# Optimization experiments

Hardware: AMD Instinct MI355X
Metric: run time of the kernel (lower is better)

The kernel has to match this reference:

```python
import jax, jax.numpy as jnp
import numpy as np
from jax import lax

D_MODEL = 384
D_INNER = 768          # expand * d_model
D_HALF = D_INNER // 2  # 384
D_STATE = 16
D_CONV = 4
DT_RANK = 24           # ceil(384/16)
BATCH = 8
SEQLEN = 4097
EXTRAS = 1
LMAIN = SEQLEN - EXTRAS


def setup_inputs() -> dict:
    key = jax.random.key(0)
    ks = jax.random.split(key, 12)
    hidden_states = jax.random.normal(ks[0], (BATCH, SEQLEN, D_MODEL), jnp.float32)
    in_proj_w = jax.random.normal(ks[1], (D_INNER, D_MODEL), jnp.float32) * 0.02
    conv_x_w = jax.random.normal(ks[2], (D_HALF, 1, D_CONV), jnp.float32) * 0.2
    conv_z_w = jax.random.normal(ks[3], (D_HALF, 1, D_CONV), jnp.float32) * 0.2
    x_proj_w = jax.random.normal(ks[4], (DT_RANK + 2 * D_STATE, D_HALF), jnp.float32) * 0.02
    dt_std = DT_RANK ** -0.5
    dt_proj_w = jax.random.uniform(ks[5], (D_HALF, DT_RANK), jnp.float32, -dt_std, dt_std)
    # bias = inverse softplus of dt sampled log-uniform in [1e-3, 1e-1]
    dt = jnp.exp(jax.random.uniform(ks[6], (D_HALF,), jnp.float32)
                 * (jnp.log(0.1) - jnp.log(0.001)) + jnp.log(0.001))
    dt = jnp.clip(dt, 1e-4, None)
    dt_proj_b = dt + jnp.log(-jnp.expm1(-dt))
    A_log = jnp.log(jnp.broadcast_to(jnp.arange(1, D_STATE + 1, dtype=jnp.float32),
                                     (D_HALF, D_STATE)))
    D_param = jnp.ones((D_HALF,), jnp.float32)
    out_proj_w = jax.random.normal(ks[7], (D_MODEL, D_HALF), jnp.float32) * 0.02
    perm = jax.random.permutation(ks[8], LMAIN).astype(jnp.int64)
    perm_rev = jnp.argsort(perm).astype(jnp.int64)
    return {
        "hidden_states": hidden_states,
        "in_proj_w": in_proj_w,
        "conv_x_w": conv_x_w,
        "conv_z_w": conv_z_w,
        "x_proj_w": x_proj_w,
        "dt_proj_w": dt_proj_w,
        "dt_proj_b": dt_proj_b,
        "A_log": A_log,
        "D_param": D_param,
        "out_proj_w": out_proj_w,
        "perm": perm,
        "perm_rev": perm_rev,
    }


def _depthwise_conv_same(x, w):
    # x: (B, C, L), w: (C, 1, K); torch padding='same' for k=4 -> pad (left=1, right=2)
    total = D_CONV - 1
    left = total // 2
    return lax.conv_general_dilated(
        x, w, window_strides=(1,), padding=[(left, total - left)],
        dimension_numbers=("NCH", "OIH", "NCH"), feature_group_count=D_HALF)


def _selective_scan(x, dt, A, Bm, Cm, D_param, delta_bias):
    # x, dt: (B, d, L); A: (d, n); Bm, Cm: (B, n, L)
    dt = jax.nn.softplus(dt + delta_bias[None, :, None])
    xT = jnp.moveaxis(x, 2, 0)    # (L, B, d)
    dtT = jnp.moveaxis(dt, 2, 0)  # (L, B, d)
    BT = jnp.moveaxis(Bm, 2, 0)   # (L, B, n)
    CT = jnp.moveaxis(Cm, 2, 0)   # (L, B, n)

    def step(h, inp):
        x_t, dt_t, B_t, C_t = inp
        dA = jnp.exp(dt_t[..., None] * A)                      # (B, d, n)
        h = h * dA + (dt_t * x_t)[..., None] * B_t[:, None, :]  # (B, d, n)
        y = jnp.einsum("bdn,bn->bd", h, C_t)
        return h, y

    h0 = jnp.zeros((x.shape[0], x.shape[1], A.shape[1]), x.dtype)
    _, ys = lax.scan(step, h0, (xT, dtT, BT, CT))
    y = jnp.moveaxis(ys, 0, 2)  # (B, d, L)
    return y + D_param[None, :, None] * x


def reference(hidden_states, in_proj_w, conv_x_w, conv_z_w, x_proj_w,
              dt_proj_w, dt_proj_b, A_log, D_param, out_proj_w, perm, perm_rev):
    # in_proj (no bias): (B,L,D) -> (B, d_inner, L)
    xz = jnp.einsum("bld,ed->bel", hidden_states, in_proj_w)
    # hilbert/zigzag reorder on the main (non-extra) tokens
    xz = jnp.concatenate([xz[:, :, :EXTRAS], xz[:, :, EXTRAS:][:, :, perm]], axis=2)

    x, z = jnp.split(xz, 2, axis=1)  # (B, d_half, L) each
    A = -jnp.exp(A_log)
    x = jax.nn.silu(_depthwise_conv_same(x, conv_x_w))
    z = jax.nn.silu(_depthwise_conv_same(z, conv_z_w))

    x_dbl = jnp.einsum("bdl,ed->bel", x, x_proj_w)  # (B, dt_rank+2n, L)
    dt_low, Bm, Cm = jnp.split(x_dbl, [DT_RANK, DT_RANK + D_STATE], axis=1)
    dt = jnp.einsum("brl,dr->bdl", dt_low, dt_proj_w)

    y = _selective_scan(x, dt, A, Bm, Cm, D_param, dt_proj_b)
    y = (y * z).transpose(0, 2, 1)  # (B, L, d_half)
    out = jnp.einsum("bld,ed->ble", y, out_proj_w)  # (B, L, D)
    # undo the permutation on the output
    out = jnp.concatenate([out[:, :EXTRAS], out[:, EXTRAS:][:, perm_rev]], axis=1)
    return out
```

## Files before the change

kernel.cpp:

```cpp
#include <hip/hip_runtime.h>
#include <hip/hip_bf16.h>

#define DEVI __device__ __forceinline__

constexpr int B_   = 8;
constexpr int L_   = 4097;
constexpr int MTOT = B_ * L_;
constexpr int DH   = 384;
constexpr int NS   = 16;
constexpr int CH   = 33;
constexpr int NCH  = (L_ + CH - 1) / CH;

typedef __bf16 bf16x8 __attribute__((ext_vector_type(8)));
typedef float  f32x4  __attribute__((ext_vector_type(4)));

DEVI float bl(unsigned v) { return __uint_as_float(v << 16); }
DEVI float bh(unsigned v) { return __uint_as_float(v & 0xffff0000u); }
DEVI float bf(const __hip_bfloat16 x) { return __bfloat162float(x); }
DEVI unsigned short f2bu(float x) {
  __hip_bfloat16 b = __float2bfloat16(x);
  return *(unsigned short*)&b;
}
DEVI float u16f(const uint4& u, int j) {
  const unsigned w = (&u.x)[j >> 1];
  return (j & 1) ? bh(w) : bl(w);
}
DEVI float softplus_f(float x) {
  return (x > 20.f) ? x : __logf(1.f + __expf(x));
}

DEVI void gld16(const __hip_bfloat16* g, __hip_bfloat16* l) {
  __builtin_amdgcn_global_load_lds(
      (const __attribute__((address_space(1))) void*)g,
      (__attribute__((address_space(3))) void*)l, 16, 0, 0);
}

__global__ void init_k(const void* hs, int* flagp,
                       const int* p0, const int* p1, int* d0, int* d1) {
  if (blockIdx.x == 0) {
    if (threadIdx.x == 0) {
      const unsigned short* u = (const unsigned short*)hs;
      int ok = 1;
      for (int i = 0; i < 8; ++i) {
        const unsigned short v = u[2 * i];
        const int e = (v >> 7) & 0xFF;
        if (!(v == 0 || (e >= 100 && e <= 140))) ok = 0;
      }
      flagp[0] = ok;
      flagp[1] = 1;
    }
    return;
  }
  __shared__ int s_or;
  const int* src = (blockIdx.x == 2) ? p1 : p0;
  int*       dst = (blockIdx.x == 2) ? d1 : d0;
  if (threadIdx.x == 0) s_or = 0;
  __syncthreads();
  int loc = 0;
  for (int i = threadIdx.x; i < 2048; i += 1024) loc |= src[2 * i + 1];
  atomicOr(&s_or, loc);
  __syncthreads();
  const bool is64 = (s_or == 0);
  for (int j = threadIdx.x; j < 4096; j += 1024)
    dst[j] = is64 ? (int)((const long long*)src)[j] : src[j];
}

struct NormSet { const void* src[8]; void* dst[8]; int n[8]; };
__global__ void norm_all(NormSet s, int* flagp,
                         const void* __restrict__ alog, float* __restrict__ a2fo) {
  const int f = flagp[0];
  if (blockIdx.x == 1152) {
    int ok = 1;
    for (int d = threadIdx.x; d < 384; d += 256) {
      float a2[16];
#pragma unroll
      for (int n = 0; n < 16; ++n) {
        const float v = f ? bf(((const __hip_bfloat16*)alog)[d * 16 + n])
                          : ((const float*)alog)[d * 16 + n];
        a2[n] = -1.4426950408889634f * __expf(v);
        a2fo[d * 16 + n] = a2[n];
      }
#pragma unroll
      for (int n = 1; n < 16; ++n) {
        const float ref = (float)(n + 1) * a2[0];
        if (fabsf(a2[n] - ref) > 1e-3f * fabsf(ref)) ok = 0;
      }
    }
    if (!ok) atomicAnd(&flagp[1], 0);
    return;
  }
  const int idx = blockIdx.x * 256 + threadIdx.x;
#pragma unroll
  for (int t = 0; t < 8; ++t) {
    if (idx < s.n[t]) {
      __hip_bfloat16* d = (__hip_bfloat16*)s.dst[t];
      if (f) d[idx] = ((const __hip_bfloat16*)s.src[t])[idx];
      else   d[idx] = __float2bfloat16(((const float*)s.src[t])[idx]);
    }
  }
}

__global__ void prep_k(const __hip_bfloat16* __restrict__ dtw,
                       const __hip_bfloat16* __restrict__ xw,
                       __hip_bfloat16* __restrict__ wcomb) {
  const int idx = blockIdx.x * 256 + threadIdx.x;
  if (idx >= 512 * 384) return;
  const int n = idx / 384, k = idx - n * 384;
  float v = 0.f;
  if (n < 384) {
#pragma unroll
    for (int r = 0; r < 24; ++r) v += bf(dtw[n * 24 + r]) * bf(xw[r * 384 + k]);
  } else if (n < 416) {
    v = bf(xw[(24 + n - 384) * 384 + k]);
  }
  wcomb[idx] = __float2bfloat16(v);
}

__global__ void cvt_k(const void* __restrict__ hs, __hip_bfloat16* __restrict__ dst,
                      const int* __restrict__ gidx, const int* __restrict__ flagp) {
  const int idx = blockIdx.x * 256 + threadIdx.x;
  if (idx >= MTOT * 48) return;
  const int j = idx % 48;
  const int r = idx / 48;
  const int b = r / L_, t = r - b * L_;
  const int src = b * L_ + (t == 0 ? 0 : 1 + gidx[t - 1]);
  uint4 o;
  if (flagp[0]) {
    o = *(const uint4*)((const __hip_bfloat16*)hs + (size_t)src * 384 + j * 8);
  } else {
    const float* f = (const float*)hs + (size_t)src * 384 + j * 8;
    const float4 f0 = *(const float4*)f;
    const float4 f1 = *(const float4*)(f + 4);
    o.x = f2bu(f0.x) | ((unsigned)f2bu(f0.y) << 16);
    o.y = f2bu(f0.z) | ((unsigned)f2bu(f0.w) << 16);
    o.z = f2bu(f1.x) | ((unsigned)f2bu(f1.y) << 16);
    o.w = f2bu(f1.z) | ((unsigned)f2bu(f1.w) << 16);
  }
  *(uint4*)(dst + (size_t)r * 384 + j * 8) = o;
}

template<int GATHER, int EPI>
__global__ __launch_bounds__(256, 4)
void gemm_k(const __hip_bfloat16* __restrict__ A, const __hip_bfloat16* __restrict__ W,
            void* __restrict__ e0, void* __restrict__ e1,
            const __hip_bfloat16* __restrict__ bias,
            const int* __restrict__ gidx, const int* __restrict__ flagp,
            int M, int N)
{
  __shared__ __align__(16) char smem[36864];
  __hip_bfloat16* lA = (__hip_bfloat16*)smem;
  __hip_bfloat16* lB = lA + 2 * 4096;
  const int tid  = threadIdx.x;
  const int lane = tid & 63;
  const int wv   = tid >> 6;
  const int wm   = wv >> 1, wn = wv & 1;
  const int lrow = lane & 15, quad = lane >> 4;
  const int fbf  = flagp[0];

  const int NT = gridDim.x;
  const int nblocks = NT * (int)gridDim.y;
  const int id = blockIdx.y * NT + blockIdx.x;
  const int q8 = nblocks >> 3, r8 = nblocks & 7;
  const int xcd = id & 7, slot = id >> 3;
  const int nid = (xcd < r8 ? xcd * (q8 + 1)
                            : r8 * (q8 + 1) + (xcd - r8) * q8) + slot;
  const int mt = nid / NT, nt = nid - mt * NT;

  const bool live = !(EPI == 1 && nt * 128 + wn * 64 >= 416);

  const __hip_bfloat16* aSrc[2];
  const __hip_bfloat16* bSrc[2];
#pragma unroll
  for (int p = 0; p < 2; ++p) {
    const int s   = p * 256 + tid;
    const int row = s >> 2;
    const int kc  = (s & 3) * 8;
    int r = mt * 128 + row;
    if (r >= M) r = M - 1;
    int src;
    if (GATHER) { const int b = r / L_, t = r - b * L_;
                  src = b * L_ + (t == 0 ? 0 : 1 + gidx[t - 1]); }
    else        { src = r; }
    aSrc[p] = A + (size_t)src * 384 + kc;
    bSrc[p] = W + (size_t)(nt * 128 + row) * 384 + kc;
  }

  auto stage = [&](int kt, int buf) {
#pragma unroll
    for (int p = 0; p < 2; ++p) {
      const int s = p * 256 + tid;
      gld16(aSrc[p] + kt * 32, &lA[buf * 4096 + s * 8]);
      gld16(bSrc[p] + kt * 32, &lB[buf * 4096 + s * 8]);
    }
  };

  f32x4 acc[4][4] = {};

  stage(0, 0);
  __syncthreads();

#pragma unroll
  for (int kt = 0; kt < 12; ++kt) {
    const int buf = kt & 1;
    if (kt < 11) stage(kt + 1, buf ^ 1);
    if (live) {
      bf16x8 af[4], bfr[4];
#pragma unroll
      for (int i = 0; i < 4; ++i)
        af[i] = *reinterpret_cast<const bf16x8*>(
            &lA[buf * 4096 + (wm * 64 + i * 16 + lrow) * 32 + quad * 8]);
#pragma unroll
      for (int j = 0; j < 4; ++j)
        bfr[j] = *reinterpret_cast<const bf16x8*>(
            &lB[buf * 4096 + (wn * 64 + j * 16 + lrow) * 32 + quad * 8]);
#pragma unroll
      for (int i = 0; i < 4; ++i)
#pragma unroll
        for (int j = 0; j < 4; ++j)
          acc[i][j] = __builtin_amdgcn_mfma_f32_16x16x32_bf16(af[i], bfr[j], acc[i][j], 0, 0, 0);
    }
    __syncthreads();
  }

  const int r0c = mt * 128;
  if (EPI == 1 && nt == 3) {
#pragma unroll
    for (int i = 0; i < 4; ++i) {
      const int row0 = r0c + wm * 64 + i * 16 + quad * 4;
#pragma unroll
      for (int j = 0; j < 4; ++j) {
        const int col = 384 + wn * 64 + j * 16 + lrow;
        if (col >= 416) continue;
#pragma unroll
        for (int rg = 0; rg < 4; ++rg) {
          const int r = row0 + rg;
          if (r >= M) continue;
          ((float*)e1)[(size_t)r * 32 + (col - 384)] = acc[i][j][rg];
        }
      }
    }
  } else if (EPI == 2 && !fbf) {
    float* lT = (float*)smem;
#pragma unroll
    for (int h = 0; h < 2; ++h) {
      __syncthreads();
      if (wn == h) {
#pragma unroll
        for (int i = 0; i < 4; ++i)
#pragma unroll
          for (int j = 0; j < 4; ++j)
#pragma unroll
            for (int rg = 0; rg < 4; ++rg)
              lT[(wm * 64 + i * 16 + quad * 4 + rg) * 72 + j * 16 + lrow] = acc[i][j][rg];
      }
      __syncthreads();
#pragma unroll
      for (int p = 0; p < 8; ++p) {
        const int ch = p * 256 + tid;
        const int row = ch >> 4, c4 = (ch & 15) * 4;
        const int r = r0c + row;
        if (r < M) {
          const float4 v = *(const float4*)&lT[row * 72 + c4];
          *(float4*)((float*)e0 + (size_t)r * 384 + nt * 128 + h * 64 + c4) = v;
        }
      }
    }
  } else {
    __hip_bfloat16* lT = (__hip_bfloat16*)smem;
#pragma unroll
    for (int h = 0; h < 2; ++h) {
      __syncthreads();
      if (wn == h) {
        float bj[4] = {};
        if (EPI == 1) {
#pragma unroll
          for (int j = 0; j < 4; ++j)
            bj[j] = bf(bias[nt * 128 + h * 64 + j * 16 + lrow]);
        }
#pragma unroll
        for (int i = 0; i < 4; ++i)
#pragma unroll
          for (int j = 0; j < 4; ++j)
#pragma unroll
            for (int rg = 0; rg < 4; ++rg) {
              float v = acc[i][j][rg];
              if (EPI == 1) v = softplus_f(v + bj[j]);
              lT[(wm * 64 + i * 16 + quad * 4 + rg) * 72 + j * 16 + lrow] =
                  __float2bfloat16(v);
            }
      }
      __syncthreads();
#pragma unroll
      for (int p = 0; p < 4; ++p) {
        const int ch = p * 256 + tid;
        const int row = ch >> 3, c8 = (ch & 7) * 8;
        const int r = r0c + row;
        if (r < M) {
          const uint4 v = *(const uint4*)&lT[row * 72 + c8];
          const int g = nt * 128 + h * 64 + c8;
          __hip_bfloat16* dst = (EPI == 0 && g >= 384)
                ? (__hip_bfloat16*)e1 + (size_t)r * 384 + (g - 384)
                : (__hip_bfloat16*)e0 + (size_t)r * 384 + g;
          *(uint4*)dst = v;
        }
      }
    }
  }
}

__global__ void convx_k(const __hip_bfloat16* __restrict__ xh,
                        const __hip_bfloat16* __restrict__ cxw,
                        __hip_bfloat16* __restrict__ xc) {
  const int idx = blockIdx.x * 256 + threadIdx.x;
  if (idx >= MTOT * 48) return;
  const int g  = idx % 48;
  const int rg = idx / 48;
  const int t  = rg % L_;
  const int c0 = g * 8;
  uint4 wv[4];
#pragma unroll
  for (int p = 0; p < 4; ++p) wv[p] = *(const uint4*)(cxw + c0 * 4 + p * 8);
  float acc[8] = {};
#pragma unroll
  for (int k = 0; k < 4; ++k) {
    const int tt = t + k - 1;
    if (tt < 0 || tt >= L_) continue;
    const uint4 u = *(const uint4*)(xh + (size_t)(rg + k - 1) * 384 + c0);
#pragma unroll
    for (int j = 0; j < 8; ++j) {
      const int e = j * 4 + k;
      acc[j] += u16f(wv[e >> 3], e & 7) * u16f(u, j);
    }
  }
  uint4 o;
#pragma unroll
  for (int p = 0; p < 4; ++p) {
    const float s0 = acc[2 * p]     / (1.f + __expf(-acc[2 * p]));
    const float s1 = acc[2 * p + 1] / (1.f + __expf(-acc[2 * p + 1]));
    (&o.x)[p] = f2bu(s0) | ((unsigned)f2bu(s1) << 16);
  }
  *(uint4*)(xc + (size_t)rg * 384 + c0) = o;
}

__global__ __launch_bounds__(128)
void scan1_k(const __hip_bfloat16* __restrict__ dt, const float* __restrict__ bc,
             __hip_bfloat16* __restrict__ xcio,
             const float* __restrict__ a2f,
             const __hip_bfloat16* __restrict__ dpar,
             float* __restrict__ pbuf, float* __restrict__ hend,
             const int* __restrict__ flagp)
{
  __shared__ __align__(16) float lBC[CH * 32];
  const int blk = blockIdx.x;
  const int dt3 = blk % 3;
  const int c   = (blk / 3) % NCH;
  const int b   = blk / (3 * NCH);
  const int d   = dt3 * 128 + threadIdx.x;
  const int t0  = c * CH;
  const int r0  = b * L_ + t0;
  const int tmax = (L_ - t0 < CH) ? (L_ - t0) : CH;
  for (int i = threadIdx.x; i < tmax * 32; i += 128) lBC[i] = bc[(size_t)r0 * 32 + i];
  __syncthreads();

  float h[16];
#pragma unroll
  for (int n = 0; n < 16; ++n) h[n] = 0.f;
  float sdt = 0.f;
  const float Dd = bf(dpar[d]);
  const size_t base = ((size_t)(c * 8 + b) * 16) * 384 + d;

  float dtv = bf(dt[(size_t)r0 * 384 + d]);
  float xv  = bf(xcio[(size_t)r0 * 384 + d]);

  if (flagp[1]) {
    const float a2b = a2f[d * 16];
    for (int tt = 0; tt < tmax; ++tt) {
      const size_t r = (size_t)(r0 + tt);
      float dtv_n = 0.f, xv_n = 0.f;
      if (tt + 1 < tmax) {
        dtv_n = bf(dt[(r + 1) * 384 + d]);
        xv_n  = bf(xcio[(r + 1) * 384 + d]);
      }
      sdt += dtv;
      const float dtx = dtv * xv;
      float pw[17];
      pw[1] = exp2f(dtv * a2b);
#pragma unroll
      for (int n = 2; n <= 16; ++n) pw[n] = pw[n >> 1] * pw[n - (n >> 1)];
      float4 bq[4], cq[4];
#pragma unroll
      for (int q = 0; q < 4; ++q) {
        bq[q] = *(const float4*)&lBC[tt * 32 + q * 4];
        cq[q] = *(const float4*)&lBC[tt * 32 + 16 + q * 4];
      }
      float ya = 0.f, yb = 0.f;
#pragma unroll
      for (int n = 0; n < 16; ++n) {
        h[n] = h[n] * pw[n + 1] + dtx * (&bq[n >> 2].x)[n & 3];
        const float t = h[n] * (&cq[n >> 2].x)[n & 3];
        if (n & 1) yb += t; else ya += t;
      }
      const float y = ya + yb + Dd * xv;
      xcio[r * 384 + d] = __float2bfloat16(y);
      dtv = dtv_n; xv = xv_n;
    }
    float Ep[17];
    Ep[1] = exp2f(sdt * a2b);
#pragma unroll
    for (int n = 2; n <= 16; ++n) Ep[n] = Ep[n >> 1] * Ep[n - (n >> 1)];
#pragma unroll
    for (int n = 0; n < 16; ++n) {
      pbuf[base + n * 384] = Ep[n + 1];
      hend[base + n * 384] = h[n];
    }
  } else {
    float a2[16];
#pragma unroll
    for (int n = 0; n < 16; ++n) a2[n] = a2f[d * 16 + n];
    for (int tt = 0; tt < tmax; ++tt) {
      const size_t r = (size_t)(r0 + tt);
      float dtv_n = 0.f, xv_n = 0.f;
      if (tt + 1 < tmax) {
        dtv_n = bf(dt[(r + 1) * 384 + d]);
        xv_n  = bf(xcio[(r + 1) * 384 + d]);
      }
      sdt += dtv;
      const float dtx = dtv * xv;
      float4 bq[4], cq[4];
#pragma unroll
      for (int q = 0; q < 4; ++q) {
        bq[q] = *(const float4*)&lBC[tt * 32 + q * 4];
        cq[q] = *(const float4*)&lBC[tt * 32 + 16 + q * 4];
      }
      float ya = 0.f, yb = 0.f;
#pragma unroll
      for (int n = 0; n < 16; ++n) {
        h[n] = h[n] * exp2f(dtv * a2[n]) + dtx * (&bq[n >> 2].x)[n & 3];
        const float t = h[n] * (&cq[n >> 2].x)[n & 3];
        if (n & 1) yb += t; else ya += t;
      }
      const float y = ya + yb + Dd * xv;
      xcio[r * 384 + d] = __float2bfloat16(y);
      dtv = dtv_n; xv = xv_n;
    }
#pragma unroll
    for (int n = 0; n < 16; ++n) {
      pbuf[base + n * 384] = exp2f(sdt * a2[n]);
      hend[base + n * 384] = h[n];
    }
  }
}

__global__ void scan2_k(float* __restrict__ pbuf, const float* __restrict__ hend) {
  const int tid = blockIdx.x * 256 + threadIdx.x;
  const int d = tid % 384;
  const int n = (tid / 384) & 15;
  const int b = tid / 6144;
  float H = 0.f;
  for (int c = 0; c < NCH; ++c) {
    const size_t idx = ((size_t)(c * 8 + b) * 16 + n) * 384 + d;
    const float p = pbuf[idx];
    const float he = hend[idx];
    pbuf[idx] = H;
    H = p * H + he;
  }
}

__global__ __launch_bounds__(128)
void scan3_k(__hip_bfloat16* __restrict__ dtyg, const float* __restrict__ bc,
             const __hip_bfloat16* __restrict__ yl,
             const __hip_bfloat16* __restrict__ zh,
             const __hip_bfloat16* __restrict__ czw,
             const float* __restrict__ a2f,
             const float* __restrict__ hstart,
             const int* __restrict__ flagp)
{
  __shared__ __align__(16) float lC[CH * 16];
  const int blk = blockIdx.x;
  const int dt3 = blk % 3;
  const int c   = (blk / 3) % NCH;
  const int b   = blk / (3 * NCH);
  const int d   = dt3 * 128 + threadIdx.x;
  const int t0  = c * CH;
  const int r0  = b * L_ + t0;
  const int tmax = (L_ - t0 < CH) ? (L_ - t0) : CH;
  for (int i = threadIdx.x; i < tmax * 16; i += 128)
    lC[i] = bc[(size_t)r0 * 32 + (i >> 4) * 32 + 16 + (i & 15)];
  __syncthreads();

  float hs_[16];
  const size_t base = ((size_t)(c * 8 + b) * 16) * 384 + d;
#pragma unroll
  for (int n = 0; n < 16; ++n) hs_[n] = hstart[base + n * 384];
  float cw[4];
#pragma unroll
  for (int k = 0; k < 4; ++k) cw[k] = bf(czw[d * 4 + k]);

  float zm1 = (t0 - 1 >= 0) ? bf(zh[(size_t)(r0 - 1) * 384 + d]) : 0.f;
  float z0  = bf(zh[(size_t)r0 * 384 + d]);
  float zp1 = (t0 + 1 < L_) ? bf(zh[(size_t)(r0 + 1) * 384 + d]) : 0.f;
  float sdt = 0.f;

  float dtv = bf(dtyg[(size_t)r0 * 384 + d]);
  float ylv = bf(yl[(size_t)r0 * 384 + d]);

  if (flagp[1]) {
    const float a2b = a2f[d * 16];
    for (int tt = 0; tt < tmax; ++tt) {
      const int t = t0 + tt;
      const size_t r = (size_t)(r0 + tt);
      const float zp2 = (t + 2 < L_) ? bf(zh[(r + 2) * 384 + d]) : 0.f;
      float dtv_n = 0.f, ylv_n = 0.f;
      if (tt + 1 < tmax) {
        dtv_n = bf(dtyg[(r + 1) * 384 + d]);
        ylv_n = bf(yl[(r + 1) * 384 + d]);
      }
      sdt += dtv;
      float pw[17];
      pw[1] = exp2f(sdt * a2b);
#pragma unroll
      for (int n = 2; n <= 16; ++n) pw[n] = pw[n >> 1] * pw[n - (n >> 1)];
      float4 cq[4];
#pragma unroll
      for (int q = 0; q < 4; ++q) cq[q] = *(const float4*)&lC[tt * 16 + q * 4];
      float ca = 0.f, cb = 0.f;
#pragma unroll
      for (int n = 0; n < 16; ++n) {
        const float t2 = (&cq[n >> 2].x)[n & 3] * hs_[n] * pw[n + 1];
        if (n & 1) cb += t2; else ca += t2;
      }
      const float y = ylv + ca + cb;
      const float zc = cw[0] * zm1 + cw[1] * z0 + cw[2] * zp1 + cw[3] * zp2;
      const float zs = zc / (1.f + __expf(-zc));
      dtyg[r * 384 + d] = __float2bfloat16(y * zs);
      zm1 = z0; z0 = zp1; zp1 = zp2;
      dtv = dtv_n; ylv = ylv_n;
    }
  } else {
    float a2[16];
#pragma unroll
    for (int n = 0; n < 16; ++n) a2[n] = a2f[d * 16 + n];
    for (int tt = 0; tt < tmax; ++tt) {
      const int t = t0 + tt;
      const size_t r = (size_t)(r0 + tt);
      const float zp2 = (t + 2 < L_) ? bf(zh[(r + 2) * 384 + d]) : 0.f;
      float dtv_n = 0.f, ylv_n = 0.f;
      if (tt + 1 < tmax) {
        dtv_n = bf(dtyg[(r + 1) * 384 + d]);
        ylv_n = bf(yl[(r + 1) * 384 + d]);
      }
      sdt += dtv;
      float4 cq[4];
#pragma unroll
      for (int q = 0; q < 4; ++q) cq[q] = *(const float4*)&lC[tt * 16 + q * 4];
      float ca = 0.f, cb = 0.f;
#pragma unroll
      for (int n = 0; n < 16; ++n) {
        const float t2 = (&cq[n >> 2].x)[n & 3] * hs_[n] * exp2f(sdt * a2[n]);
        if (n & 1) cb += t2; else ca += t2;
      }
      const float y = ylv + ca + cb;
      const float zc = cw[0] * zm1 + cw[1] * z0 + cw[2] * zp1 + cw[3] * zp2;
      const float zs = zc / (1.f + __expf(-zc));
      dtyg[r * 384 + d] = __float2bfloat16(y * zs);
      zm1 = z0; z0 = zp1; zp1 = zp2;
      dtv = dtv_n; ylv = ylv_n;
    }
  }
}

extern "C" void kernel_launch(void* const* d_in, const int* in_sizes, int n_in,
                              void* d_out, int out_size, void* d_ws, size_t ws_size,
                              hipStream_t stream) {
  const void* hs   = d_in[0];
  const void* w_in = d_in[1];
  const void* cxw  = d_in[2];
  const void* czw  = d_in[3];
  const void* xw   = d_in[4];
  const void* dtw  = d_in[5];
  const void* dtb  = d_in[6];
  const void* alog = d_in[7];
  const void* dpar = d_in[8];
  const void* ow   = d_in[9];
  const int* perm  = (const int*)d_in[10];
  const int* permr = (const int*)d_in[11];

  char* ws = (char*)d_ws;
  size_t off = 0;
  auto alloc = [&](size_t nbytes) -> char* {
    char* p = ws + off;
    off += (nbytes + 255) & ~(size_t)255;
    return p;
  };
  int* flag              = (int*)alloc(256);
  int* nperm             = (int*)alloc(4096 * 4);
  int* npermr            = (int*)alloc(4096 * 4);
  float* a2f             = (float*)alloc(6144 * 4);
  __hip_bfloat16* w_inb  = (__hip_bfloat16*)alloc(294912 * 2);
  __hip_bfloat16* cxwb   = (__hip_bfloat16*)alloc(1536 * 2);
  __hip_bfloat16* czwb   = (__hip_bfloat16*)alloc(1536 * 2);
  __hip_bfloat16* xwb    = (__hip_bfloat16*)alloc(21504 * 2);
  __hip_bfloat16* dtwb   = (__hip_bfloat16*)alloc(9216 * 2);
  __hip_bfloat16* dtbb   = (__hip_bfloat16*)alloc(384 * 2);
  __hip_bfloat16* dparb  = (__hip_bfloat16*)alloc(384 * 2);
  __hip_bfloat16* owb    = (__hip_bfloat16*)alloc(147456 * 2);
  __hip_bfloat16* wcombb = (__hip_bfloat16*)alloc((size_t)512 * 384 * 2);
  __hip_bfloat16* hsb    = (__hip_bfloat16*)alloc((size_t)MTOT * 384 * 2);
  __hip_bfloat16* zh     = (__hip_bfloat16*)alloc((size_t)MTOT * 384 * 2);
  __hip_bfloat16* xc     = (__hip_bfloat16*)alloc((size_t)MTOT * 384 * 2);
  __hip_bfloat16* dtyg   = (__hip_bfloat16*)alloc((size_t)MTOT * 384 * 2);
  float*          bcf    = (float*)alloc((size_t)MTOT * 32 * 4);
  __hip_bfloat16* xh   = (__hip_bfloat16*)d_out;
  float*          pbuf = (float*)d_out;
  float*          hend = (float*)((char*)d_out + (size_t)NCH * B_ * NS * DH * 4);

  init_k<<<3, 1024, 0, stream>>>(hs, flag, perm, permr, nperm, npermr);
  NormSet ns;
  ns.src[0] = w_in; ns.dst[0] = w_inb; ns.n[0] = 294912;
  ns.src[1] = ow;   ns.dst[1] = owb;   ns.n[1] = 147456;
  ns.src[2] = xw;   ns.dst[2] = xwb;   ns.n[2] = 21504;
  ns.src[3] = dtw;  ns.dst[3] = dtwb;  ns.n[3] = 9216;
  ns.src[4] = cxw;  ns.dst[4] = cxwb;  ns.n[4] = 1536;
  ns.src[5] = czw;  ns.dst[5] = czwb;  ns.n[5] = 1536;
  ns.src[6] = dtb;  ns.dst[6] = dtbb;  ns.n[6] = 384;
  ns.src[7] = dpar; ns.dst[7] = dparb; ns.n[7] = 384;
  norm_all<<<1153, 256, 0, stream>>>(ns, flag, alog, a2f);
  prep_k<<<768, 256, 0, stream>>>(dtwb, xwb, wcombb);
  cvt_k<<<(MTOT * 48 + 255) / 256, 256, 0, stream>>>(hs, hsb, nperm, flag);
  gemm_k<0, 0><<<dim3(6, 257), 256, 0, stream>>>(
      hsb, w_inb, xh, zh, nullptr, nullptr, flag, MTOT, 768);
  convx_k<<<(MTOT * 48 + 255) / 256, 256, 0, stream>>>(xh, cxwb, xc);
  gemm_k<0, 1><<<dim3(4, 257), 256, 0, stream>>>(
      xc, wcombb, dtyg, bcf, dtbb, nullptr, flag, MTOT, 512);
  scan1_k<<<B_ * NCH * 3, 128, 0, stream>>>(dtyg, bcf, xc, a2f, dparb, pbuf, hend, flag);
  scan2_k<<<192, 256, 0, stream>>>(pbuf, hend);
  scan3_k<<<B_ * NCH * 3, 128, 0, stream>>>(dtyg, bcf, xc, zh, czwb, a2f, pbuf, flag);
  gemm_k<1, 2><<<dim3(3, 257), 256, 0, stream>>>(
      dtyg, owb, d_out, nullptr, nullptr, npermr, flag, MTOT, 384);
  (void)in_sizes; (void)n_in; (void)out_size; (void)ws_size;
}
```

Before: 334.4 us.

## Fuse input conversion and gather into in_proj GEMM; merge setup kernels

Removes the separate cvt_k pass, which gathered and converted the hidden states to a bf16 buffer. The in_proj GEMM now loads fp32 (or bf16) rows directly through registers with the permutation gather, converts them and writes them to LDS. It also merges init_k, norm_all and prep_k into one setup kernel that probes the dtype per block, cutting three launches to one. The trade-off is that the A operand no longer uses the async global_load_lds path, so the conversion adds register pressure and latency inside the GEMM loop.

```diff
diff --git a/kernel.cpp b/kernel.cpp
--- a/kernel.cpp
+++ b/kernel.cpp
@@ -28,6 +28,17 @@
 DEVI float softplus_f(float x) {
   return (x > 20.f) ? x : __logf(1.f + __expf(x));
 }
+DEVI int probe_bf16(const void* hs) {
+  const unsigned short* u = (const unsigned short*)hs;
+  int ok = 1;
+#pragma unroll
+  for (int i = 0; i < 8; ++i) {
+    const unsigned short v = u[2 * i];
+    const int e = (v >> 7) & 0xFF;
+    if (!(v == 0 || (e >= 100 && e <= 140))) ok = 0;
+  }
+  return ok;
+}
 
 DEVI void gld16(const __hip_bfloat16* g, __hip_bfloat16* l) {
   __builtin_amdgcn_global_load_lds(
@@ -35,41 +46,32 @@
       (__attribute__((address_space(3))) void*)l, 16, 0, 0);
 }
 
-__global__ void init_k(const void* hs, int* flagp,
-                       const int* p0, const int* p1, int* d0, int* d1) {
-  if (blockIdx.x == 0) {
-    if (threadIdx.x == 0) {
-      const unsigned short* u = (const unsigned short*)hs;
-      int ok = 1;
-      for (int i = 0; i < 8; ++i) {
-        const unsigned short v = u[2 * i];
-        const int e = (v >> 7) & 0xFF;
-        if (!(v == 0 || (e >= 100 && e <= 140))) ok = 0;
-      }
-      flagp[0] = ok;
-      flagp[1] = 1;
+struct NormSet { const void* src[6]; void* dst[6]; int n[6]; };
+__global__ void setup_k(const void* hs, int* flagp,
+                        const int* p0, const int* p1, int* d0, int* d1,
+                        NormSet s, const void* __restrict__ alog,
+                        float* __restrict__ a2fo,
+                        const void* __restrict__ dtw, const void* __restrict__ xw,
+                        __hip_bfloat16* __restrict__ wcomb) {
+  const int bid = blockIdx.x;
+  const int f = probe_bf16(hs);
+
+  if (bid < 1152) {
+    const int idx = bid * 256 + threadIdx.x;
+#pragma unroll
+    for (int t = 0; t < 6; ++t) {
+      if (idx < s.n[t]) {
+        __hip_bfloat16* d = (__hip_bfloat16*)s.dst[t];
+        if (f) d[idx] = ((const __hip_bfloat16*)s.src[t])[idx];
+        else   d[idx] = __float2bfloat16(((const float*)s.src[t])[idx]);
+      }
     }
     return;
   }
-  __shared__ int s_or;
-  const int* src = (blockIdx.x == 2) ? p1 : p0;
-  int*       dst = (blockIdx.x == 2) ? d1 : d0;
-  if (threadIdx.x == 0) s_or = 0;
-  __syncthreads();
-  int loc = 0;
-  for (int i = threadIdx.x; i < 2048; i += 1024) loc |= src[2 * i + 1];
-  atomicOr(&s_or, loc);
-  __syncthreads();
-  const bool is64 = (s_or == 0);
-  for (int j = threadIdx.x; j < 4096; j += 1024)
-    dst[j] = is64 ? (int)((const long long*)src)[j] : src[j];
-}
-
-struct NormSet { const void* src[8]; void* dst[8]; int n[8]; };
-__global__ void norm_all(NormSet s, int* flagp,
-                         const void* __restrict__ alog, float* __restrict__ a2fo) {
-  const int f = flagp[0];
-  if (blockIdx.x == 1152) {
+  if (bid == 1152) {
+    __shared__ int s_ok;
+    if (threadIdx.x == 0) s_ok = 1;
+    __syncthreads();
     int ok = 1;
     for (int d = threadIdx.x; d < 384; d += 256) {
       float a2[16];
@@ -86,62 +88,46 @@
         if (fabsf(a2[n] - ref) > 1e-3f * fabsf(ref)) ok = 0;
       }
     }
-    if (!ok) atomicAnd(&flagp[1], 0);
+    if (!ok) atomicAnd(&s_ok, 0);
+    __syncthreads();
+    if (threadIdx.x == 0) { flagp[0] = f; flagp[1] = s_ok; }
     return;
   }
-  const int idx = blockIdx.x * 256 + threadIdx.x;
-#pragma unroll
-  for (int t = 0; t < 8; ++t) {
-    if (idx < s.n[t]) {
-      __hip_bfloat16* d = (__hip_bfloat16*)s.dst[t];
-      if (f) d[idx] = ((const __hip_bfloat16*)s.src[t])[idx];
-      else   d[idx] = __float2bfloat16(((const float*)s.src[t])[idx]);
-    }
-  }
-}
-
-__global__ void prep_k(const __hip_bfloat16* __restrict__ dtw,
-                       const __hip_bfloat16* __restrict__ xw,
-                       __hip_bfloat16* __restrict__ wcomb) {
-  const int idx = blockIdx.x * 256 + threadIdx.x;
+  if (bid <= 1154) {
+    __shared__ int s_or;
+    const int* src = (bid == 1154) ? p1 : p0;
+    int*       dst = (bid == 1154) ? d1 : d0;
+    if (threadIdx.x == 0) s_or = 0;
+    __syncthreads();
+    int loc = 0;
+    for (int i = threadIdx.x; i < 2048; i += 256) loc |= src[2 * i + 1];
+    atomicOr(&s_or, loc);
+    __syncthreads();
+    const bool is64 = (s_or == 0);
+    for (int j = threadIdx.x; j < 4096; j += 256)
+      dst[j] = is64 ? (int)((const long long*)src)[j] : src[j];
+    return;
+  }
+  const int idx = (bid - 1155) * 256 + threadIdx.x;
   if (idx >= 512 * 384) return;
   const int n = idx / 384, k = idx - n * 384;
+  auto rd = [&](const void* w, int i) -> float {
+    return f ? bf(((const __hip_bfloat16*)w)[i])
+             : bf(__float2bfloat16(((const float*)w)[i]));
+  };
   float v = 0.f;
   if (n < 384) {
 #pragma unroll
-    for (int r = 0; r < 24; ++r) v += bf(dtw[n * 24 + r]) * bf(xw[r * 384 + k]);
+    for (int r = 0; r < 24; ++r) v += rd(dtw, n * 24 + r) * rd(xw, r * 384 + k);
   } else if (n < 416) {
-    v = bf(xw[(24 + n - 384) * 384 + k]);
+    v = rd(xw, (24 + n - 384) * 384 + k);
   }
   wcomb[idx] = __float2bfloat16(v);
 }
 
-__global__ void cvt_k(const void* __restrict__ hs, __hip_bfloat16* __restrict__ dst,
-                      const int* __restrict__ gidx, const int* __restrict__ flagp) {
-  const int idx = blockIdx.x * 256 + threadIdx.x;
-  if (idx >= MTOT * 48) return;
-  const int j = idx % 48;
-  const int r = idx / 48;
-  const int b = r / L_, t = r - b * L_;
-  const int src = b * L_ + (t == 0 ? 0 : 1 + gidx[t - 1]);
-  uint4 o;
-  if (flagp[0]) {
-    o = *(const uint4*)((const __hip_bfloat16*)hs + (size_t)src * 384 + j * 8);
-  } else {
-    const float* f = (const float*)hs + (size_t)src * 384 + j * 8;
-    const float4 f0 = *(const float4*)f;
-    const float4 f1 = *(const float4*)(f + 4);
-    o.x = f2bu(f0.x) | ((unsigned)f2bu(f0.y) << 16);
-    o.y = f2bu(f0.z) | ((unsigned)f2bu(f0.w) << 16);
-    o.z = f2bu(f1.x) | ((unsigned)f2bu(f1.y) << 16);
-    o.w = f2bu(f1.z) | ((unsigned)f2bu(f1.w) << 16);
-  }
-  *(uint4*)(dst + (size_t)r * 384 + j * 8) = o;
-}
-
-template<int GATHER, int EPI>
+template<int AFP, int GATHER, int EPI>
 __global__ __launch_bounds__(256, 4)
-void gemm_k(const __hip_bfloat16* __restrict__ A, const __hip_bfloat16* __restrict__ W,
+void gemm_k(const void* __restrict__ Av, const __hip_bfloat16* __restrict__ W,
             void* __restrict__ e0, void* __restrict__ e1,
             const __hip_bfloat16* __restrict__ bias,
             const int* __restrict__ gidx, const int* __restrict__ flagp,
@@ -168,7 +154,7 @@
 
   const bool live = !(EPI == 1 && nt * 128 + wn * 64 >= 416);
 
-  const __hip_bfloat16* aSrc[2];
+  size_t aOff[2];
   const __hip_bfloat16* bSrc[2];
 #pragma unroll
   for (int p = 0; p < 2; ++p) {
@@ -181,28 +167,67 @@
     if (GATHER) { const int b = r / L_, t = r - b * L_;
                   src = b * L_ + (t == 0 ? 0 : 1 + gidx[t - 1]); }
     else        { src = r; }
-    aSrc[p] = A + (size_t)src * 384 + kc;
+    aOff[p] = (size_t)src * 384 + kc;
     bSrc[p] = W + (size_t)(nt * 128 + row) * 384 + kc;
   }
 
-  auto stage = [&](int kt, int buf) {
+  float4 fA0[2], fA1[2];
+  uint4  uA[2];
+
+  auto issueA = [&](int kt) {
+    if (AFP) {
+      if (fbf) {
+#pragma unroll
+        for (int p = 0; p < 2; ++p)
+          uA[p] = *(const uint4*)((const __hip_bfloat16*)Av + aOff[p] + kt * 32);
+      } else {
+#pragma unroll
+        for (int p = 0; p < 2; ++p) {
+          const float* fp = (const float*)Av + aOff[p] + kt * 32;
+          fA0[p] = *(const float4*)fp;
+          fA1[p] = *(const float4*)(fp + 4);
+        }
+      }
+    }
+  };
+  auto writeA = [&](int buf) {
+    if (AFP) {
+#pragma unroll
+      for (int p = 0; p < 2; ++p) {
+        uint4 w;
+        if (fbf) {
+          w = uA[p];
+        } else {
+          w.x = f2bu(fA0[p].x) | ((unsigned)f2bu(fA0[p].y) << 16);
+          w.y = f2bu(fA0[p].z) | ((unsigned)f2bu(fA0[p].w) << 16);
+          w.z = f2bu(fA1[p].x) | ((unsigned)f2bu(fA1[p].y) << 16);
+          w.w = f2bu(fA1[p].z) | ((unsigned)f2bu(fA1[p].w) << 16);
+        }
+        *(uint4*)&lA[buf * 4096 + (p * 256 + tid) * 8] = w;
+      }
+    }
+  };
+  auto stageHW = [&](int kt, int buf) {
 #pragma unroll
     for (int p = 0; p < 2; ++p) {
       const int s = p * 256 + tid;
-      gld16(aSrc[p] + kt * 32, &lA[buf * 4096 + s * 8]);
+      if (!AFP)
+        gld16((const __hip_bfloat16*)Av + aOff[p] + kt * 32, &lA[buf * 4096 + s * 8]);
       gld16(bSrc[p] + kt * 32, &lB[buf * 4096 + s * 8]);
     }
   };
 
   f32x4 acc[4][4] = {};
 
-  stage(0, 0);
+  issueA(0);
+  stageHW(0, 0);
+  writeA(0);
   __syncthreads();
 
 #pragma unroll
   for (int kt = 0; kt < 12; ++kt) {
     const int buf = kt & 1;
-    if (kt < 11) stage(kt + 1, buf ^ 1);
+    if (kt < 11) { issueA(kt + 1); stageHW(kt + 1, buf ^ 1); }
     if (live) {
       bf16x8 af[4], bfr[4];
 #pragma unroll
@@ -219,6 +244,7 @@
         for (int j = 0; j < 4; ++j)
           acc[i][j] = __builtin_amdgcn_mfma_f32_16x16x32_bf16(af[i], bfr[j], acc[i][j], 0, 0, 0);
     }
+    if (kt < 11) writeA(buf ^ 1);
     __syncthreads();
   }
 
@@ -599,13 +625,10 @@
   __hip_bfloat16* w_inb  = (__hip_bfloat16*)alloc(294912 * 2);
   __hip_bfloat16* cxwb   = (__hip_bfloat16*)alloc(1536 * 2);
   __hip_bfloat16* czwb   = (__hip_bfloat16*)alloc(1536 * 2);
-  __hip_bfloat16* xwb    = (__hip_bfloat16*)alloc(21504 * 2);
-  __hip_bfloat16* dtwb   = (__hip_bfloat16*)alloc(9216 * 2);
   __hip_bfloat16* dtbb   = (__hip_bfloat16*)alloc(384 * 2);
   __hip_bfloat16* dparb  = (__hip_bfloat16*)alloc(384 * 2);
   __hip_bfloat16* owb    = (__hip_bfloat16*)alloc(147456 * 2);
   __hip_bfloat16* wcombb = (__hip_bfloat16*)alloc((size_t)512 * 384 * 2);
-  __hip_bfloat16* hsb    = (__hip_bfloat16*)alloc((size_t)MTOT * 384 * 2);
   __hip_bfloat16* zh     = (__hip_bfloat16*)alloc((size_t)MTOT * 384 * 2);
   __hip_bfloat16* xc     = (__hip_bfloat16*)alloc((size_t)MTOT * 384 * 2);
   __hip_bfloat16* dtyg   = (__hip_bfloat16*)alloc((size_t)MTOT * 384 * 2);
@@ -614,28 +637,24 @@
   float*          pbuf = (float*)d_out;
   float*          hend = (float*)((char*)d_out + (size_t)NCH * B_ * NS * DH * 4);
 
-  init_k<<<3, 1024, 0, stream>>>(hs, flag, perm, permr, nperm, npermr);
   NormSet ns;
   ns.src[0] = w_in; ns.dst[0] = w_inb; ns.n[0] = 294912;
   ns.src[1] = ow;   ns.dst[1] = owb;   ns.n[1] = 147456;
-  ns.src[2] = xw;   ns.dst[2] = xwb;   ns.n[2] = 21504;
-  ns.src[3] = dtw;  ns.dst[3] = dtwb;  ns.n[3] = 9216;
-  ns.src[4] = cxw;  ns.dst[4] = cxwb;  ns.n[4] = 1536;
-  ns.src[5] = czw;  ns.dst[5] = czwb;  ns.n[5] = 1536;
-  ns.src[6] = dtb;  ns.dst[6] = dtbb;  ns.n[6] = 384;
-  ns.src[7] = dpar; ns.dst[7] = dparb; ns.n[7] = 384;
-  norm_all<<<1153, 256, 0, stream>>>(ns, flag, alog, a2f);
-  prep_k<<<768, 256, 0, stream>>>(dtwb, xwb, wcombb);
-  cvt_k<<<(MTOT * 48 + 255) / 256, 256, 0, stream>>>(hs, hsb, nperm, flag);
-  gemm_k<0, 0><<<dim3(6, 257), 256, 0, stream>>>(
-      hsb, w_inb, xh, zh, nullptr, nullptr, flag, MTOT, 768);
+  ns.src[2] = cxw;  ns.dst[2] = cxwb;  ns.n[2] = 1536;
+  ns.src[3] = czw;  ns.dst[3] = czwb;  ns.n[3] = 1536;
+  ns.src[4] = dtb;  ns.dst[4] = dtbb;  ns.n[4] = 384;
+  ns.src[5] = dpar; ns.dst[5] = dparb; ns.n[5] = 384;
+  setup_k<<<1923, 256, 0, stream>>>(hs, flag, perm, permr, nperm, npermr,
+                                    ns, alog, a2f, dtw, xw, wcombb);
+  gemm_k<1, 1, 0><<<dim3(6, 257), 256, 0, stream>>>(
+      hs, w_inb, xh, zh, nullptr, nperm, flag, MTOT, 768);
   convx_k<<<(MTOT * 48 + 255) / 256, 256, 0, stream>>>(xh, cxwb, xc);
-  gemm_k<0, 1><<<dim3(4, 257), 256, 0, stream>>>(
+  gemm_k<0, 0, 1><<<dim3(4, 257), 256, 0, stream>>>(
       xc, wcombb, dtyg, bcf, dtbb, nullptr, flag, MTOT, 512);
   scan1_k<<<B_ * NCH * 3, 128, 0, stream>>>(dtyg, bcf, xc, a2f, dparb, pbuf, hend, flag);
   scan2_k<<<192, 256, 0, stream>>>(pbuf, hend);
   scan3_k<<<B_ * NCH * 3, 128, 0, stream>>>(dtyg, bcf, xc, zh, czwb, a2f, pbuf, flag);
-  gemm_k<1, 2><<<dim3(3, 257), 256, 0, stream>>>(
+  gemm_k<0, 1, 2><<<dim3(3, 257), 256, 0, stream>>>(
       dtyg, owb, d_out, nullptr, nullptr, npermr, flag, MTOT, 384);
   (void)in_sizes; (void)n_in; (void)out_size; (void)ws_size;
 }
```

After: 402.4 us. 20.3% more time.
